# Kernel tuning notes

Hardware: AMD Instinct MI355X
Metric: run time of the kernel (lower is better)

## Reference

```python
import jax, jax.numpy as jnp
import numpy as np
import math

# ---- static configuration (mirrors init_kwargs) ----
NQ = 8            # n_qubits (main register)
NA = 2            # n_ancilla = ceil(log2(n_select))
NSEL = 4          # n_select
DEG = 3           # degree
LAYERS = 2        # n_ansatz_layers
KLOC = 2          # k_local
LATENT = 128
B = 256
NROTS = 4 * NQ * LAYERS          # 64
GROUPS = [(s, s + 1) for s in range(NQ - KLOC + 1)]  # sliding 2-local -> 7 groups
NOBS = len(GROUPS)
KDIM = 2 ** KLOC                  # 4
C64 = jnp.complex64
TWO_PI = 2.0 * math.pi

CNOT = jnp.array([[1, 0, 0, 0], [0, 1, 0, 0], [0, 0, 0, 1], [0, 0, 1, 0]], dtype=C64)

# ---- gate matrices (theta may be traced) ----
def ry_mat(th):
    c = jnp.cos(th / 2).astype(C64); s = jnp.sin(th / 2).astype(C64)
    return jnp.stack([jnp.stack([c, -s]), jnp.stack([s, c])])

def rz_mat(th):
    return jnp.diag(jnp.stack([jnp.exp(-0.5j * th), jnp.exp(0.5j * th)])).astype(C64)

def crx_mat(th):
    c = jnp.cos(th / 2).astype(C64); isn = (-1j * jnp.sin(th / 2)).astype(C64)
    one = jnp.ones((), C64)
    m = jnp.zeros((4, 4), C64)
    m = m.at[0, 0].set(one).at[1, 1].set(one)
    m = m.at[2, 2].set(c).at[3, 3].set(c).at[2, 3].set(isn).at[3, 2].set(isn)
    return m

# ---- state-vector gate application (state: (2,)*rank, wire = axis) ----
def apply_1q(state, U, w):
    return jnp.moveaxis(jnp.tensordot(U, state, axes=((1,), (w,))), 0, w)

def apply_2q(state, U, w0, w1):
    st = jnp.tensordot(U.reshape(2, 2, 2, 2), state, axes=((2, 3), (w0, w1)))
    return jnp.moveaxis(st, (0, 1), (w0, w1))

def _sim14_ops(nq, layers):
    ops, idx = [], 0
    for _ in range(layers):
        for i in range(nq):
            ops.append(("ry", (i,), idx)); idx += 1
        for i in range(nq - 1, -1, -1):
            ops.append(("crx", (i, (i + 1) % nq), idx)); idx += 1
        for i in range(nq):
            ops.append(("ry", (i,), idx)); idx += 1
        for i in [nq - 1] + list(range(nq - 1)):
            ops.append(("crx", (i, (i - 1) % nq), idx)); idx += 1
    return ops

def apply_sim14(state, p, layers, adjoint=False):
    ops = _sim14_ops(NQ, layers)
    seq = list(reversed(ops)) if adjoint else ops
    sgn = -1.0 if adjoint else 1.0
    for kind, ws, idx in seq:
        th = sgn * p[idx]
        if kind == "ry":
            state = apply_1q(state, ry_mat(th), ws[0])
        else:
            state = apply_2q(state, crx_mat(th), ws[0], ws[1])
    return state

def pcphase(state, phi):
    # e^{+i phi} on ancilla=|0..0> subspace (first 2^NQ states in (anc, main) ordering), e^{-i phi} elsewhere
    sr = state.reshape(2 ** NQ, 2 ** NA)
    ph = jnp.where(jnp.arange(2 ** NA) == 0, jnp.exp(1j * phi), jnp.exp(-1j * phi)).astype(C64)
    return (sr * ph[None, :]).reshape(state.shape)

def prepare(state, prep_p, adjoint=False):
    if not adjoint:
        for ly in range(NA):          # n_prep_layers == n_ancilla
            for qi in range(NA):
                state = apply_1q(state, ry_mat(prep_p[ly, qi, 0]), NQ + qi)
                state = apply_1q(state, rz_mat(prep_p[ly, qi, 1]), NQ + qi)
            for i in range(NA - 1):
                state = apply_2q(state, CNOT, NQ + i, NQ + i + 1)
    else:
        for ly in reversed(range(NA)):
            for i in reversed(range(NA - 1)):
                state = apply_2q(state, CNOT, NQ + i, NQ + i + 1)
            for qi in reversed(range(NA)):
                state = apply_1q(state, rz_mat(-prep_p[ly, qi, 1]), NQ + qi)
                state = apply_1q(state, ry_mat(-prep_p[ly, qi, 0]), NQ + qi)
    return state

def select(state, ts, adjoint=False):
    # ancilla wires (NQ, NQ+1) are the trailing axes; flattened index == control value s
    sr = state.reshape((2,) * NQ + (2 ** NA,))
    for s in range(NSEL):
        sub = apply_sim14(sr[..., s], ts[s], LAYERS, adjoint=adjoint)
        sr = sr.at[..., s].set(sub)
    return sr.reshape(state.shape)

def create_hermitian(A, Bp, D, N):
    h = jnp.zeros((N, N), C64)
    count = 0
    for i in range(1, N):
        h = h.at[i - 1, i - 1].set(D[i].astype(C64))
        for j in range(i):
            h = h.at[i, j].set((A[count + j] + 1j * Bp[count + j]).astype(C64))
        count += i
    return h + h.conj().T

def simulate(ts, prep_p, sig, qff, H_all):
    # ts: (NSEL, NROTS) for one batch element
    state = jnp.zeros((2,) * (NQ + NA), C64).at[(0,) * (NQ + NA)].set(1.0)
    state = pcphase(state, sig[0])
    for k in range(DEG):
        state = prepare(state, prep_p)
        state = select(state, ts, adjoint=(k % 2 == 1))
        state = prepare(state, prep_p, adjoint=True)
        state = pcphase(state, sig[k + 1])
    state = apply_sim14(state, qff, 1)
    es = []
    for w, (a, b) in enumerate(GROUPS):
        hpsi = apply_2q(state, H_all[w], a, b)
        es.append(jnp.real(jnp.vdot(state, hpsi)))
    return jnp.stack(es).astype(jnp.float32)  # (NOBS,)

def linear(x, w, b):
    return x @ w.T + b

def sinusoidal_embedding(t, dim):
    half = dim // 2
    freqs = jnp.exp(-math.log(10000.0) * jnp.arange(half, dtype=jnp.float32) / half)
    args = t[:, None] * freqs[None]
    return jnp.concatenate([jnp.cos(args), jnp.sin(args)], axis=-1)

def _forward(z_t, t, te_w1, te_b1, te_w2, te_b2, ip_w1, ip_b1, ip_w2, ip_b2,
             prep_params, signal_angles, qff_params, A_obs, B_obs, D_obs, head_w, head_b):
    t_emb = sinusoidal_embedding(t, LATENT)
    t_emb = linear(jax.nn.silu(linear(t_emb, te_w1, te_b1)), te_w2, te_b2)
    h = jnp.concatenate([z_t, t_emb], axis=-1)
    h = linear(jax.nn.silu(linear(h, ip_w1, ip_b1)), ip_w2, ip_b2)
    ts = jax.nn.sigmoid(h).reshape(z_t.shape[0], NSEL, NROTS) * TWO_PI
    H_all = jax.vmap(lambda a, b, d: create_hermitian(a, b, d, KDIM))(A_obs, B_obs, D_obs)  # (NOBS,4,4)
    expvals = jax.vmap(simulate, in_axes=(0, None, None, None, None))(
        ts, prep_params, signal_angles, qff_params, H_all)  # (B, NOBS)
    return linear(expvals, head_w, head_b)  # (B, LATENT)

def setup_inputs() -> dict:
    key = jax.random.key(0)
    ks = jax.random.split(key, 16)
    def n(k, shape, s=0.05):
        return s * jax.random.normal(k, shape, jnp.float32)
    return {
        "z_t": jax.random.normal(ks[0], (B, LATENT), jnp.float32),
        "t": jax.random.uniform(ks[1], (B,), jnp.float32),
        "te_w1": n(ks[2], (LATENT, LATENT)), "te_b1": jnp.zeros((LATENT,), jnp.float32),
        "te_w2": n(ks[3], (LATENT, LATENT)), "te_b2": jnp.zeros((LATENT,), jnp.float32),
        "ip_w1": n(ks[4], (2 * LATENT, 2 * LATENT)), "ip_b1": jnp.zeros((2 * LATENT,), jnp.float32),
        "ip_w2": n(ks[5], (NSEL * NROTS, 2 * LATENT)), "ip_b2": jnp.zeros((NSEL * NROTS,), jnp.float32),
        "prep_params": 0.1 * jax.random.normal(ks[6], (NA, NA, 2), jnp.float32),
        "signal_angles": 0.1 * jax.random.normal(ks[7], (DEG + 1,), jnp.float32),
        "qff_params": jax.random.uniform(ks[8], (4 * NQ,), jnp.float32),
        "A_obs": 2.0 * jax.random.normal(ks[9], (NOBS, KDIM * (KDIM - 1) // 2), jnp.float32),
        "B_obs": 2.0 * jax.random.normal(ks[10], (NOBS, KDIM * (KDIM - 1) // 2), jnp.float32),
        "D_obs": 2.0 * jax.random.normal(ks[11], (NOBS, KDIM), jnp.float32),
        "head_w": n(ks[12], (LATENT, NOBS)), "head_b": jnp.zeros((LATENT,), jnp.float32),
    }

def reference(z_t, t, te_w1, te_b1, te_w2, te_b2, ip_w1, ip_b1, ip_w2, ip_b2,
              prep_params, signal_angles, qff_params, A_obs, B_obs, D_obs, head_w, head_b):
    return _forward(z_t, t, te_w1, te_b1, te_w2, te_b2, ip_w1, ip_b1, ip_w2, ip_b2,
                    prep_params, signal_angles, qff_params, A_obs, B_obs, D_obs, head_w, head_b)
```

## Files before the change

kernel.cpp:

```cpp
#include <hip/hip_runtime.h>
#include <math.h>

#define NOBS 7
#define PI_F 3.14159265358979f


template<int LM>
__device__ __forceinline__ float lane_partner(float x) {
  if constexpr (LM == 1) {
    return __int_as_float(__builtin_amdgcn_mov_dpp(__float_as_int(x), 0xB1, 0xF, 0xF, true));
  } else if constexpr (LM == 2) {
    return __int_as_float(__builtin_amdgcn_mov_dpp(__float_as_int(x), 0x4E, 0xF, 0xF, true));
  } else if constexpr (LM == 4) {
    int a = __builtin_amdgcn_mov_dpp(__float_as_int(x), 0x1B, 0xF, 0xF, true);
    return __int_as_float(__builtin_amdgcn_mov_dpp(a, 0x141, 0xF, 0xF, true));
  } else if constexpr (LM == 8) {
    int a = __builtin_amdgcn_mov_dpp(__float_as_int(x), 0x141, 0xF, 0xF, true);
    return __int_as_float(__builtin_amdgcn_mov_dpp(a, 0x140, 0xF, 0xF, true));
  } else if constexpr (LM == 16) {
#if __has_builtin(__builtin_amdgcn_permlane16_swap)
    unsigned xu = __float_as_uint(x);
    auto r = __builtin_amdgcn_permlane16_swap(xu, xu, false, false);
    return (__uint_as_float(r[0]) + __uint_as_float(r[1])) - x;
#else
// ... 35 lines not shown

__device__ __forceinline__ float rdlane(float v, int idx) {
  return __int_as_float(__builtin_amdgcn_readlane(__float_as_int(v), idx));
}

__device__ __forceinline__ float2 cmul(float2 a, float2 b) {
  return make_float2(a.x*b.x - a.y*b.y, a.x*b.y + a.y*b.x);
}
__device__ __forceinline__ float2 cmulc(float2 a, float2 b) {
  return make_float2(a.x*b.x + a.y*b.y, a.y*b.x - a.x*b.y);
}
__device__ __forceinline__ float2 cadd(float2 a, float2 b) {
  return make_float2(a.x + b.x, a.y + b.y);
}

struct S4 { float r0, r1, i0, i1; };

__device__ __forceinline__ float4 wexch(int pp, int wv, int lane,
                                        const float* vr, const float* vi) {
  extern __shared__ float4 dxw[];
  float4* buf = dxw + pp * 512;
  buf[wv * 64 + lane] = make_float4(vr[0], vr[1], vi[0], vi[1]);
  __syncthreads();
  return buf[(wv ^ 4) * 64 + lane];
}


template<int W>
__device__ __forceinline__ void ry_lane_g(float* vr, float* vi, int lane,
                                          float ct, float st, int idx, float sg) {
  float c = rdlane(ct, idx), s = sg * rdlane(st, idx);
  constexpr int LM = 1 << (5 - W);
  const float ls = (lane & LM) ? s : -s;
#pragma unroll
  for (int r = 0; r < 2; ++r) {
    float pr = lane_partner<LM>(vr[r]);
    float pi = lane_partner<LM>(vi[r]);
    vr[r] = c*vr[r] + ls*pr;
    vi[r] = c*vi[r] + ls*pi;
  }
}

__device__ __forceinline__ void ry_wave6_g(float* vr, float* vi, int wv, int lane, int h,
                                           float ct, float st, int idx, float sg, int pp) {
  float c = rdlane(ct, idx), s = sg * rdlane(st, idx);
  float4 P = wexch(pp, wv, lane, vr, vi);
  const float ls = h ? s : -s;
  vr[0] = c*vr[0] + ls*P.x;  vr[1] = c*vr[1] + ls*P.y;
  vi[0] = c*vi[0] + ls*P.z;  vi[1] = c*vi[1] + ls*P.w;
}

__device__ __forceinline__ void ry_reg7_g(float* vr, float* vi,
                                          float ct, float st, int idx, float sg) {
  float c = rdlane(ct, idx), s = sg * rdlane(st, idx);
  float a0 = vr[0], a1 = vr[1];
  vr[0] = c*a0 - s*a1;  vr[1] = s*a0 + c*a1;
  float b0 = vi[0], b1 = vi[1];
  vi[0] = c*b0 - s*b1;  vi[1] = s*b0 + c*b1;
}

template<int C, int T>
__device__ __forceinline__ void crx_ll_g(float* vr, float* vi, int lane,
                                         float ct, float st, int idx, float sg) {
  float c = rdlane(ct, idx), s = sg * rdlane(st, idx);
  constexpr int LC = 1 << (5 - C), LT = 1 << (5 - T);
  const bool act = (lane & LC) != 0;
  const float cp = act ? c : 1.f, sp = act ? s : 0.f;
#pragma unroll
  for (int r = 0; r < 2; ++r) {
    float pr = lane_partner<LT>(vr[r]);
    float pi = lane_partner<LT>(vi[r]);
    vr[r] = cp*vr[r] + sp*pi;
    vi[r] = cp*vi[r] - sp*pr;
  }
}

template<int T>
__device__ __forceinline__ void crx_7l_g(float* vr, float* vi,
                                         float ct, float st, int idx, float sg) {
  float c = rdlane(ct, idx), s = sg * rdlane(st, idx);
  constexpr int LT = 1 << (5 - T);
  float pr = lane_partner<LT>(vr[1]);
  float pi = lane_partner<LT>(vi[1]);
  vr[1] = c*vr[1] + s*pi;
  vi[1] = c*vi[1] - s*pr;
}

template<int C>
__device__ __forceinline__ void crx_l7_g(float* vr, float* vi, int lane,
                                         float ct, float st, int idx, float sg) {
  float c = rdlane(ct, idx), s = sg * rdlane(st, idx);
  constexpr int LC = 1 << (5 - C);
  const bool act = (lane & LC) != 0;
  const float cp = act ? c : 1.f, sp = act ? s : 0.f;
  float xr = vr[0], xi = vi[0], yr = vr[1], yi = vi[1];
  vr[0] = cp*xr + sp*yi;  vi[0] = cp*xi - sp*yr;
  vr[1] = cp*yr + sp*xi;  vi[1] = cp*yi - sp*xr;
}

template<int C>
__device__ __forceinline__ void crx_l6_g(float* vr, float* vi, int wv, int lane,
                                         float ct, float st, int idx, float sg, int pp) {
  float c = rdlane(ct, idx), s = sg * rdlane(st, idx);
  float4 P = wexch(pp, wv, lane, vr, vi);
  constexpr int LC = 1 << (5 - C);
  const bool act = (lane & LC) != 0;
  const float cp = act ? c : 1.f, sp = act ? s : 0.f;
  vr[0] = cp*vr[0] + sp*P.z;  vi[0] = cp*vi[0] - sp*P.x;
  vr[1] = cp*vr[1] + sp*P.w;  vi[1] = cp*vi[1] - sp*P.y;
}

__device__ __forceinline__ void crx_76_g(float* vr, float* vi, int wv, int lane,
                                         float ct, float st, int idx, float sg, int pp) {
  float c = rdlane(ct, idx), s = sg * rdlane(st, idx);
  float4 P = wexch(pp, wv, lane, vr, vi);
  vr[1] = c*vr[1] + s*P.w;
  vi[1] = c*vi[1] - s*P.y;
}

__device__ __forceinline__ void crx_67_g(float* vr, float* vi, int h,
                                         float ct, float st, int idx, float sg) {
  if (h) {
    float c = rdlane(ct, idx), s = sg * rdlane(st, idx);
    float xr = vr[0], xi = vi[0], yr = vr[1], yi = vi[1];
    vr[0] = c*xr + s*yi;  vi[0] = c*xi - s*yr;
    vr[1] = c*yr + s*xi;  vi[1] = c*yi - s*xr;
  }
}

template<int T>
__device__ __forceinline__ void crx_6l_g(float* vr, float* vi, int h,
                                         float ct, float st, int idx, float sg) {
  if (h) {
    float c = rdlane(ct, idx), s = sg * rdlane(st, idx);
    constexpr int LT = 1 << (5 - T);
#pragma unroll
    for (int r = 0; r < 2; ++r) {
      float pr = lane_partner<LT>(vr[r]);
      float pi = lane_partner<LT>(vi[r]);
      vr[r] = c*vr[r] + s*pi;
      vi[r] = c*vi[r] - s*pr;
    }
  }
}


__device__ __noinline__ S4 sim14_fwd(S4 v, float ct, float st, int off) {
  const int tid = threadIdx.x;
  const int lane = tid & 63, wv = tid >> 6, h = wv >> 2;
  float vr[2] = {v.r0, v.r1}, vi[2] = {v.i0, v.i1};
  const float sg = 1.f;
  ry_lane_g<0>(vr,vi,lane,ct,st,off+0,sg); ry_lane_g<1>(vr,vi,lane,ct,st,off+1,sg);
  ry_lane_g<2>(vr,vi,lane,ct,st,off+2,sg); ry_lane_g<3>(vr,vi,lane,ct,st,off+3,sg);
  ry_lane_g<4>(vr,vi,lane,ct,st,off+4,sg); ry_lane_g<5>(vr,vi,lane,ct,st,off+5,sg);
  ry_wave6_g(vr,vi,wv,lane,h,ct,st,off+6,sg,0);
  ry_reg7_g(vr,vi,ct,st,off+7,sg);
  crx_7l_g<0>(vr,vi,ct,st,off+8,sg);
  crx_67_g(vr,vi,h,ct,st,off+9,sg);
  crx_l6_g<5>(vr,vi,wv,lane,ct,st,off+10,sg,1);
  crx_ll_g<4,5>(vr,vi,lane,ct,st,off+11,sg); crx_ll_g<3,4>(vr,vi,lane,ct,st,off+12,sg);
  crx_ll_g<2,3>(vr,vi,lane,ct,st,off+13,sg); crx_ll_g<1,2>(vr,vi,lane,ct,st,off+14,sg);
  crx_ll_g<0,1>(vr,vi,lane,ct,st,off+15,sg);
  ry_lane_g<0>(vr,vi,lane,ct,st,off+16,sg); ry_lane_g<1>(vr,vi,lane,ct,st,off+17,sg);
  ry_lane_g<2>(vr,vi,lane,ct,st,off+18,sg); ry_lane_g<3>(vr,vi,lane,ct,st,off+19,sg);
  ry_lane_g<4>(vr,vi,lane,ct,st,off+20,sg); ry_lane_g<5>(vr,vi,lane,ct,st,off+21,sg);
  ry_wave6_g(vr,vi,wv,lane,h,ct,st,off+22,sg,0);
  ry_reg7_g(vr,vi,ct,st,off+23,sg);
  crx_76_g(vr,vi,wv,lane,ct,st,off+24,sg,1);
  crx_l7_g<0>(vr,vi,lane,ct,st,off+25,sg);
  crx_ll_g<1,0>(vr,vi,lane,ct,st,off+26,sg); crx_ll_g<2,1>(vr,vi,lane,ct,st,off+27,sg);
  crx_ll_g<3,2>(vr,vi,lane,ct,st,off+28,sg); crx_ll_g<4,3>(vr,vi,lane,ct,st,off+29,sg);
  crx_ll_g<5,4>(vr,vi,lane,ct,st,off+30,sg);
  crx_6l_g<5>(vr,vi,h,ct,st,off+31,sg);
  return {vr[0], vr[1], vi[0], vi[1]};
}

__device__ __noinline__ S4 sim14_adj(S4 v, float ct, float st, int off) {
  const int tid = threadIdx.x;
  const int lane = tid & 63, wv = tid >> 6, h = wv >> 2;
  float vr[2] = {v.r0, v.r1}, vi[2] = {v.i0, v.i1};
  const float sg = -1.f;
  crx_6l_g<5>(vr,vi,h,ct,st,off+31,sg);
  crx_ll_g<5,4>(vr,vi,lane,ct,st,off+30,sg); crx_ll_g<4,3>(vr,vi,lane,ct,st,off+29,sg);
  crx_ll_g<3,2>(vr,vi,lane,ct,st,off+28,sg); crx_ll_g<2,1>(vr,vi,lane,ct,st,off+27,sg);
  crx_ll_g<1,0>(vr,vi,lane,ct,st,off+26,sg);
  crx_l7_g<0>(vr,vi,lane,ct,st,off+25,sg);
  crx_76_g(vr,vi,wv,lane,ct,st,off+24,sg,0);
  ry_reg7_g(vr,vi,ct,st,off+23,sg);
  ry_wave6_g(vr,vi,wv,lane,h,ct,st,off+22,sg,1);
  ry_lane_g<5>(vr,vi,lane,ct,st,off+21,sg); ry_lane_g<4>(vr,vi,lane,ct,st,off+20,sg);
  ry_lane_g<3>(vr,vi,lane,ct,st,off+19,sg); ry_lane_g<2>(vr,vi,lane,ct,st,off+18,sg);
  ry_lane_g<1>(vr,vi,lane,ct,st,off+17,sg); ry_lane_g<0>(vr,vi,lane,ct,st,off+16,sg);
  crx_ll_g<0,1>(vr,vi,lane,ct,st,off+15,sg); crx_ll_g<1,2>(vr,vi,lane,ct,st,off+14,sg);
  crx_ll_g<2,3>(vr,vi,lane,ct,st,off+13,sg); crx_ll_g<3,4>(vr,vi,lane,ct,st,off+12,sg);
  crx_ll_g<4,5>(vr,vi,lane,ct,st,off+11,sg);
  crx_l6_g<5>(vr,vi,wv,lane,ct,st,off+10,sg,0);
  crx_67_g(vr,vi,h,ct,st,off+9,sg);
  crx_7l_g<0>(vr,vi,ct,st,off+8,sg);
  ry_reg7_g(vr,vi,ct,st,off+7,sg);
  ry_wave6_g(vr,vi,wv,lane,h,ct,st,off+6,sg,1);
  ry_lane_g<5>(vr,vi,lane,ct,st,off+5,sg); ry_lane_g<4>(vr,vi,lane,ct,st,off+4,sg);
  ry_lane_g<3>(vr,vi,lane,ct,st,off+3,sg); ry_lane_g<2>(vr,vi,lane,ct,st,off+2,sg);
  ry_lane_g<1>(vr,vi,lane,ct,st,off+1,sg); ry_lane_g<0>(vr,vi,lane,ct,st,off+0,sg);
  return {vr[0], vr[1], vi[0], vi[1]};
}


__global__ void setup_kernel(const float* __restrict__ prep_p,
                             const float* __restrict__ sig,
                             const float* __restrict__ qff,
                             float* __restrict__ ws) {
  const int t = threadIdx.x;
  float2 Ga[2][2][2], Gb[2][2][2];
  for (int ly = 0; ly < 2; ++ly)
    for (int qi = 0; qi < 2; ++qi) {
      float y = prep_p[ly*4 + qi*2 + 0], z = prep_p[ly*4 + qi*2 + 1];
      float cy, sy, cz, sz;
      __sincosf(0.5f*y, &sy, &cy);
      __sincosf(0.5f*z, &sz, &cz);
// ... 80 lines not shown
      if constexpr (MODE == 0) {
        yl[row] = a / (1.f + __expf(-a));
      } else if constexpr (MODE == 1) {
        yl[row] = a;
      } else {
        float th = PI_F / (1.f + __expf(-a));
        float sn, cn;
        __sincosf(th, &sn, &cn);
        ((float2*)yl)[row] = make_float2(cn, sn);
      }
    }
  }
}


__global__ __launch_bounds__(512) void qsvt_kernel(
    const float* __restrict__ z_t, const float* __restrict__ t,
    const float* __restrict__ te_w1, const float* __restrict__ te_b1,
    const float* __restrict__ te_w2, const float* __restrict__ te_b2,
    const float* __restrict__ ip_w1, const float* __restrict__ ip_b1,
    const float* __restrict__ ip_w2, const float* __restrict__ ip_b2,
    const float* __restrict__ A_obs, const float* __restrict__ B_obs,
    const float* __restrict__ D_obs,
    const float* __restrict__ head_w, const float* __restrict__ head_b,
    const float* __restrict__ ws,
    float* __restrict__ out)
{
  __shared__ __align__(16) float emb[128];
  __shared__ __align__(16) float y1[128];
  __shared__ __align__(16) float hbuf[256];
  __shared__ __align__(16) float h1[256];
  __shared__ __align__(16) float2 seltab[256];
  __shared__ __align__(16) float2 xanc[128 * 9];
  __shared__ __align__(16) float dumpR[4][256];
  __shared__ __align__(16) float dumpI[4][256];
  __shared__ float redbuf[NOBS][4];
  __shared__ float hdc[NOBS][3], hxc[NOBS][6], hyc[NOBS][6];
  __shared__ __align__(16) float shw[128 * NOBS];
  __shared__ __align__(16) float shb[128];

  const int tid  = threadIdx.x;
  const int lane = tid & 63;
  const int wv   = tid >> 6;
  const int s    = wv & 3;
  const int h    = wv >> 2;
  const int b    = blockIdx.x;

  if (tid < 128) {
    float fr = ws[168 + (tid & 63)];
    float arg = t[b] * fr;
    float sn, cn;
    __sincosf(arg, &sn, &cn);
    emb[tid] = (tid < 64) ? cn : sn;
  }
  __syncthreads();

  mlp_layer<128, 2, 0>(te_w1, te_b1, emb, y1, wv * 16, lane);
  if (tid < 128) hbuf[tid] = z_t[b * 128 + tid];
  __syncthreads();

  mlp_layer<128, 2, 1>(te_w2, te_b2, y1, hbuf + 128, wv * 16, lane);
  __syncthreads();

  mlp_layer<256, 4, 0>(ip_w1, ip_b1, hbuf, h1, wv * 32, lane);
  __syncthreads();

  mlp_layer<256, 4, 2>(ip_w2, ip_b2, h1, (float*)seltab, wv * 32, lane);

  if (tid < NOBS * 6)      { hxc[tid/6][tid%6] = A_obs[tid]; hyc[tid/6][tid%6] = B_obs[tid]; }
  else if (tid >= 64 && tid < 64 + NOBS*3) { int q = tid - 64; hdc[q/3][q%3] = 2.f * D_obs[(q/3)*4 + (q%3) + 1]; }
#pragma unroll
  for (int i = tid; i < 128*NOBS; i += 512) shw[i] = head_w[i];
  if (tid < 128) shb[tid] = head_b[tid];
  __syncthreads();

  float2 mycs = seltab[(s << 6) | lane];
  float selc = mycs.x, sels = mycs.y;
  float2 myq = ((const float2*)(ws + 104))[lane & 31];
  float qc = myq.x, qs = myq.y;

  S4 v;
  v.r0 = 0.f; v.r1 = 0.f; v.i0 = 0.f; v.i1 = 0.f;
  if (lane == 0 && h == 0) {
    float2 a0 = ((const float2*)(ws + 96))[s];
    v.r0 = a0.x; v.i0 = a0.y;
  }

  const int ancbase = (h * 64 + lane) * 9;

  v = sim14_fwd(v, selc, sels, 0);
  v = sim14_fwd(v, selc, sels, 32);
  {
    const float2* R = (const float2*)ws + (s << 2);
    xanc[ancbase + 0 + s] = make_float2(v.r0, v.i0);
    xanc[ancbase + 4 + s] = make_float2(v.r1, v.i1);
    __syncthreads();
    float2 o0 = cmul(R[0], xanc[ancbase + 0]);
    o0 = cadd(o0, cmul(R[1], xanc[ancbase + 1]));
    o0 = cadd(o0, cmul(R[2], xanc[ancbase + 2]));
    o0 = cadd(o0, cmul(R[3], xanc[ancbase + 3]));
    float2 o1 = cmul(R[0], xanc[ancbase + 4]);
    o1 = cadd(o1, cmul(R[1], xanc[ancbase + 5]));
    o1 = cadd(o1, cmul(R[2], xanc[ancbase + 6]));
    o1 = cadd(o1, cmul(R[3], xanc[ancbase + 7]));
    v.r0 = o0.x; v.i0 = o0.y; v.r1 = o1.x; v.i1 = o1.y;
    __syncthreads();
  }
  v = sim14_adj(v, selc, sels, 32);
  v = sim14_adj(v, selc, sels, 0);
  {
    const float2* R = (const float2*)(ws + 32) + (s << 2);
    xanc[ancbase + 0 + s] = make_float2(v.r0, v.i0);
    xanc[ancbase + 4 + s] = make_float2(v.r1, v.i1);
    __syncthreads();
    float2 o0 = cmul(R[0], xanc[ancbase + 0]);
    o0 = cadd(o0, cmul(R[1], xanc[ancbase + 1]));
    o0 = cadd(o0, cmul(R[2], xanc[ancbase + 2]));
    o0 = cadd(o0, cmul(R[3], xanc[ancbase + 3]));
    float2 o1 = cmul(R[0], xanc[ancbase + 4]);
    o1 = cadd(o1, cmul(R[1], xanc[ancbase + 5]));
    o1 = cadd(o1, cmul(R[2], xanc[ancbase + 6]));
    o1 = cadd(o1, cmul(R[3], xanc[ancbase + 7]));
    v.r0 = o0.x; v.i0 = o0.y; v.r1 = o1.x; v.i1 = o1.y;
    __syncthreads();
  }
  v = sim14_fwd(v, selc, sels, 0);
  v = sim14_fwd(v, selc, sels, 32);
  {
    const float2* R = (const float2*)(ws + 64) + (s << 2);
    xanc[ancbase + 0 + s] = make_float2(v.r0, v.i0);
    xanc[ancbase + 4 + s] = make_float2(v.r1, v.i1);
    __syncthreads();
    float2 o0 = cmul(R[0], xanc[ancbase + 0]);
    o0 = cadd(o0, cmul(R[1], xanc[ancbase + 1]));
    o0 = cadd(o0, cmul(R[2], xanc[ancbase + 2]));
    o0 = cadd(o0, cmul(R[3], xanc[ancbase + 3]));
    float2 o1 = cmul(R[0], xanc[ancbase + 4]);
    o1 = cadd(o1, cmul(R[1], xanc[ancbase + 5]));
    o1 = cadd(o1, cmul(R[2], xanc[ancbase + 6]));
    o1 = cadd(o1, cmul(R[3], xanc[ancbase + 7]));
    v.r0 = o0.x; v.i0 = o0.y; v.r1 = o1.x; v.i1 = o1.y;
    __syncthreads();
  }
  v = sim14_fwd(v, qc, qs, 0);

  *(float2*)&dumpR[s][(lane << 2) | (h << 1)] = make_float2(v.r0, v.r1);
  *(float2*)&dumpI[s][(lane << 2) | (h << 1)] = make_float2(v.i0, v.i1);
  __syncthreads();

  const int w0 = h ? 4 : 0, w1 = h ? NOBS : 4;
  for (int w = w0; w < w1; ++w) {
    const int pb = 6 - w;
    int g = lane;
    int ib = ((g >> pb) << (pb + 2)) | (g & ((1 << pb) - 1));
    float xr[4], xi[4];
#pragma unroll
    for (int i = 0; i < 4; ++i) { xr[i] = dumpR[s][ib + (i << pb)]; xi[i] = dumpI[s][ib + (i << pb)]; }
    float a = hdc[w][0] * (xr[0]*xr[0] + xi[0]*xi[0])
            + hdc[w][1] * (xr[1]*xr[1] + xi[1]*xi[1])
            + hdc[w][2] * (xr[2]*xr[2] + xi[2]*xi[2]);
    const int oi[6] = {1, 2, 2, 3, 3, 3};
    const int oj[6] = {0, 0, 1, 0, 1, 2};
#pragma unroll
    for (int k2 = 0; k2 < 6; ++k2) {
      int i = oi[k2], j = oj[k2];
      float rr = xr[i]*xr[j] + xi[i]*xi[j];
      float ii = xr[i]*xi[j] - xi[i]*xr[j];
      a += 2.f * (hxc[w][k2]*rr - hyc[w][k2]*ii);
    }
    a = xor_sum<32>(a);
    a = xor_sum<16>(a);
    a = xor_sum<8>(a);
    a = xor_sum<4>(a);
    a = xor_sum<2>(a);
    a = xor_sum<1>(a);
    if (lane == 0) redbuf[w][s] = a;
  }
  __syncthreads();

  if (tid < 128) {
    float acc = shb[tid];
#pragma unroll
    for (int w = 0; w < NOBS; ++w) {
      float ev = redbuf[w][0] + redbuf[w][1] + redbuf[w][2] + redbuf[w][3];
      acc += ev * shw[tid*NOBS + w];
    }
    out[b * 128 + tid] = acc;
  }
}

extern "C" void kernel_launch(void* const* d_in, const int* in_sizes, int n_in,
                              void* d_out, int out_size, void* d_ws, size_t ws_size,
                              hipStream_t stream) {
  (void)n_in; (void)out_size; (void)ws_size;
  const float* z_t    = (const float*)d_in[0];
  const float* t      = (const float*)d_in[1];
  const float* te_w1  = (const float*)d_in[2];
  const float* te_b1  = (const float*)d_in[3];
  const float* te_w2  = (const float*)d_in[4];
// ... 4 lines not shown
  const float* ip_b2  = (const float*)d_in[9];
  const float* prep_p = (const float*)d_in[10];
  const float* sig    = (const float*)d_in[11];
  const float* qff    = (const float*)d_in[12];
  const float* A_obs  = (const float*)d_in[13];
  const float* B_obs  = (const float*)d_in[14];
  const float* D_obs  = (const float*)d_in[15];
  const float* head_w = (const float*)d_in[16];
  const float* head_b = (const float*)d_in[17];
  float* out = (float*)d_out;
  float* ws  = (float*)d_ws;

  setup_kernel<<<1, 64, 0, stream>>>(prep_p, sig, qff, ws);

  int B = in_sizes[1];
  qsvt_kernel<<<B, 512, 2 * 512 * sizeof(float4), stream>>>(
      z_t, t, te_w1, te_b1, te_w2, te_b2, ip_w1, ip_b1, ip_w2, ip_b2,
      A_obs, B_obs, D_obs, head_w, head_b, ws, out);
}
```

Baseline: 127.4 us.

## Double block size to one amplitude per thread with padded LDS exchange

The block grows from 512 to 1024 threads, so each thread holds one complex amplitude instead of two. Qubits 6 and 7 now live across wave groups, and the two RY rotations on them are fused into one LDS exchange with a padded stride of 17 to avoid bank conflicts. Exchanges alternate between two buffers, the MLP layers are re-split across 16 waves, and the observable reduction is spread over more waves. This doubles parallelism per sample, but the added cross-wave gates need more block-wide barriers, and those barriers across 16 waves may cost more than the extra threads save.

```diff
diff --git a/kernel.cpp b/kernel.cpp
--- a/kernel.cpp
+++ b/kernel.cpp
@@ -73,195 +73,201 @@
   return make_float2(a.x + b.x, a.y + b.y);
 }
 
-struct S4 { float r0, r1, i0, i1; };
-
-__device__ __forceinline__ float4 wexch(int pp, int wv, int lane,
-                                        const float* vr, const float* vi) {
-  extern __shared__ float4 dxw[];
-  float4* buf = dxw + pp * 512;
-  buf[wv * 64 + lane] = make_float4(vr[0], vr[1], vi[0], vi[1]);
-  __syncthreads();
-  return buf[(wv ^ 4) * 64 + lane];
-}
-
-
-template<int W>
-__device__ __forceinline__ void ry_lane_g(float* vr, float* vi, int lane,
-                                          float ct, float st, int idx, float sg) {
-  float c = rdlane(ct, idx), s = sg * rdlane(st, idx);
-  constexpr int LM = 1 << (5 - W);
-  const float ls = (lane & LM) ? s : -s;
-#pragma unroll
-  for (int r = 0; r < 2; ++r) {
-    float pr = lane_partner<LM>(vr[r]);
-    float pi = lane_partner<LM>(vi[r]);
-    vr[r] = c*vr[r] + ls*pr;
-    vi[r] = c*vi[r] + ls*pi;
-  }
-}
-
-__device__ __forceinline__ void ry_wave6_g(float* vr, float* vi, int wv, int lane, int h,
-                                           float ct, float st, int idx, float sg, int pp) {
-  float c = rdlane(ct, idx), s = sg * rdlane(st, idx);
-  float4 P = wexch(pp, wv, lane, vr, vi);
-  const float ls = h ? s : -s;
-  vr[0] = c*vr[0] + ls*P.x;  vr[1] = c*vr[1] + ls*P.y;
-  vi[0] = c*vi[0] + ls*P.z;  vi[1] = c*vi[1] + ls*P.w;
-}
-
-__device__ __forceinline__ void ry_reg7_g(float* vr, float* vi,
-                                          float ct, float st, int idx, float sg) {
-  float c = rdlane(ct, idx), s = sg * rdlane(st, idx);
-  float a0 = vr[0], a1 = vr[1];
-  vr[0] = c*a0 - s*a1;  vr[1] = s*a0 + c*a1;
-  float b0 = vi[0], b1 = vi[1];
-  vi[0] = c*b0 - s*b1;  vi[1] = s*b0 + c*b1;
-}
-
-template<int C, int T>
-__device__ __forceinline__ void crx_ll_g(float* vr, float* vi, int lane,
-                                         float ct, float st, int idx, float sg) {
-  float c = rdlane(ct, idx), s = sg * rdlane(st, idx);
-  constexpr int LC = 1 << (5 - C), LT = 1 << (5 - T);
-  const bool act = (lane & LC) != 0;
-  const float cp = act ? c : 1.f, sp = act ? s : 0.f;
-#pragma unroll
-  for (int r = 0; r < 2; ++r) {
-    float pr = lane_partner<LT>(vr[r]);
-    float pi = lane_partner<LT>(vi[r]);
-    vr[r] = cp*vr[r] + sp*pi;
-    vi[r] = cp*vi[r] - sp*pr;
-  }
-}
-
-template<int T>
-__device__ __forceinline__ void crx_7l_g(float* vr, float* vi,
-                                         float ct, float st, int idx, float sg) {
-  float c = rdlane(ct, idx), s = sg * rdlane(st, idx);
-  constexpr int LT = 1 << (5 - T);
-  float pr = lane_partner<LT>(vr[1]);
-  float pi = lane_partner<LT>(vi[1]);
-  vr[1] = c*vr[1] + s*pi;
-  vi[1] = c*vi[1] - s*pr;
-}
-
-template<int C>
-__device__ __forceinline__ void crx_l7_g(float* vr, float* vi, int lane,
-                                         float ct, float st, int idx, float sg) {
-  float c = rdlane(ct, idx), s = sg * rdlane(st, idx);
-  constexpr int LC = 1 << (5 - C);
-  const bool act = (lane & LC) != 0;
-  const float cp = act ? c : 1.f, sp = act ? s : 0.f;
-  float xr = vr[0], xi = vi[0], yr = vr[1], yi = vi[1];
-  vr[0] = cp*xr + sp*yi;  vi[0] = cp*xi - sp*yr;
-  vr[1] = cp*yr + sp*xi;  vi[1] = cp*yi - sp*xr;
-}
-
-template<int C>
-__device__ __forceinline__ void crx_l6_g(float* vr, float* vi, int wv, int lane,
-                                         float ct, float st, int idx, float sg, int pp) {
-  float c = rdlane(ct, idx), s = sg * rdlane(st, idx);
-  float4 P = wexch(pp, wv, lane, vr, vi);
-  constexpr int LC = 1 << (5 - C);
-  const bool act = (lane & LC) != 0;
-  const float cp = act ? c : 1.f, sp = act ? s : 0.f;
-  vr[0] = cp*vr[0] + sp*P.z;  vi[0] = cp*vi[0] - sp*P.x;
-  vr[1] = cp*vr[1] + sp*P.w;  vi[1] = cp*vi[1] - sp*P.y;
-}
-
-__device__ __forceinline__ void crx_76_g(float* vr, float* vi, int wv, int lane,
-                                         float ct, float st, int idx, float sg, int pp) {
-  float c = rdlane(ct, idx), s = sg * rdlane(st, idx);
-  float4 P = wexch(pp, wv, lane, vr, vi);
-  vr[1] = c*vr[1] + s*P.w;
-  vi[1] = c*vi[1] - s*P.y;
-}
-
-__device__ __forceinline__ void crx_67_g(float* vr, float* vi, int h,
-                                         float ct, float st, int idx, float sg) {
-  if (h) {
-    float c = rdlane(ct, idx), s = sg * rdlane(st, idx);
-    float xr = vr[0], xi = vi[0], yr = vr[1], yi = vi[1];
-    vr[0] = c*xr + s*yi;  vi[0] = c*xi - s*yr;
-    vr[1] = c*yr + s*xi;  vi[1] = c*yi - s*xr;
-  }
-}
-
-template<int T>
-__device__ __forceinline__ void crx_6l_g(float* vr, float* vi, int h,
-                                         float ct, float st, int idx, float sg) {
-  if (h) {
-    float c = rdlane(ct, idx), s = sg * rdlane(st, idx);
-    constexpr int LT = 1 << (5 - T);
-#pragma unroll
-    for (int r = 0; r < 2; ++r) {
-      float pr = lane_partner<LT>(vr[r]);
-      float pi = lane_partner<LT>(vi[r]);
-      vr[r] = c*vr[r] + s*pi;
-      vi[r] = c*vi[r] - s*pr;
-    }
-  }
-}
-
-
-__device__ __noinline__ S4 sim14_fwd(S4 v, float ct, float st, int off) {
+struct S2 { float r, i; };
+
+#define XSLOTS 1088
+
+
+__device__ __noinline__ S2 sim14_fwd(S2 v, float ct, float st, int off, int site0) {
+  extern __shared__ float2 dxw[];
   const int tid = threadIdx.x;
-  const int lane = tid & 63, wv = tid >> 6, h = wv >> 2;
-  float vr[2] = {v.r0, v.r1}, vi[2] = {v.i0, v.i1};
+  const int lane = tid & 63, wv = tid >> 6;
+  const int s = wv & 3, q = wv >> 2;
+  const int h6 = q & 1, h7 = q >> 1;
+  const int sb = lane * 17 + s * 4;
+  float vr = v.r, vi = v.i;
   const float sg = 1.f;
-  ry_lane_g<0>(vr,vi,lane,ct,st,off+0,sg); ry_lane_g<1>(vr,vi,lane,ct,st,off+1,sg);
-  ry_lane_g<2>(vr,vi,lane,ct,st,off+2,sg); ry_lane_g<3>(vr,vi,lane,ct,st,off+3,sg);
-  ry_lane_g<4>(vr,vi,lane,ct,st,off+4,sg); ry_lane_g<5>(vr,vi,lane,ct,st,off+5,sg);
-  ry_wave6_g(vr,vi,wv,lane,h,ct,st,off+6,sg,0);
-  ry_reg7_g(vr,vi,ct,st,off+7,sg);
-  crx_7l_g<0>(vr,vi,ct,st,off+8,sg);
-  crx_67_g(vr,vi,h,ct,st,off+9,sg);
-  crx_l6_g<5>(vr,vi,wv,lane,ct,st,off+10,sg,1);
-  crx_ll_g<4,5>(vr,vi,lane,ct,st,off+11,sg); crx_ll_g<3,4>(vr,vi,lane,ct,st,off+12,sg);
-  crx_ll_g<2,3>(vr,vi,lane,ct,st,off+13,sg); crx_ll_g<1,2>(vr,vi,lane,ct,st,off+14,sg);
-  crx_ll_g<0,1>(vr,vi,lane,ct,st,off+15,sg);
-  ry_lane_g<0>(vr,vi,lane,ct,st,off+16,sg); ry_lane_g<1>(vr,vi,lane,ct,st,off+17,sg);
-  ry_lane_g<2>(vr,vi,lane,ct,st,off+18,sg); ry_lane_g<3>(vr,vi,lane,ct,st,off+19,sg);
-  ry_lane_g<4>(vr,vi,lane,ct,st,off+20,sg); ry_lane_g<5>(vr,vi,lane,ct,st,off+21,sg);
-  ry_wave6_g(vr,vi,wv,lane,h,ct,st,off+22,sg,0);
-  ry_reg7_g(vr,vi,ct,st,off+23,sg);
-  crx_76_g(vr,vi,wv,lane,ct,st,off+24,sg,1);
-  crx_l7_g<0>(vr,vi,lane,ct,st,off+25,sg);
-  crx_ll_g<1,0>(vr,vi,lane,ct,st,off+26,sg); crx_ll_g<2,1>(vr,vi,lane,ct,st,off+27,sg);
-  crx_ll_g<3,2>(vr,vi,lane,ct,st,off+28,sg); crx_ll_g<4,3>(vr,vi,lane,ct,st,off+29,sg);
-  crx_ll_g<5,4>(vr,vi,lane,ct,st,off+30,sg);
-  crx_6l_g<5>(vr,vi,h,ct,st,off+31,sg);
-  return {vr[0], vr[1], vi[0], vi[1]};
-}
-
-__device__ __noinline__ S4 sim14_adj(S4 v, float ct, float st, int off) {
+
+  auto RYL = [&](auto Wc, int idx) {
+    constexpr int LM = 1 << (5 - decltype(Wc)::value);
+    float c = rdlane(ct, idx), ss = sg * rdlane(st, idx);
+    float ls = (lane & LM) ? ss : -ss;
+    float pr = lane_partner<LM>(vr), pi = lane_partner<LM>(vi);
+    vr = c*vr + ls*pr;  vi = c*vi + ls*pi;
+  };
+  auto QUAD = [&](int i6, int i7, int site) {
+    float c6 = rdlane(ct, i6), s6 = sg * rdlane(st, i6);
+    float c7 = rdlane(ct, i7), s7 = sg * rdlane(st, i7);
+    float r60 = h6 ? s6 : c6, r61 = h6 ? c6 : -s6;
+    float r70 = h7 ? s7 : c7, r71 = h7 ? c7 : -s7;
+    float2* buf = dxw + (site & 1) * XSLOTS;
+    buf[sb + q] = make_float2(vr, vi);
+    __syncthreads();
+    float2 p0 = buf[sb+0], p1 = buf[sb+1], p2 = buf[sb+2], p3 = buf[sb+3];
+    float f0 = r60*r70, f1 = r61*r70, f2 = r60*r71, f3 = r61*r71;
+    vr = f0*p0.x + f1*p1.x + f2*p2.x + f3*p3.x;
+    vi = f0*p0.y + f1*p1.y + f2*p2.y + f3*p3.y;
+  };
+  auto CRXLL = [&](auto Cc, auto Tc, int idx) {
+    constexpr int LC = 1 << (5 - decltype(Cc)::value);
+    constexpr int LT = 1 << (5 - decltype(Tc)::value);
+    float c = rdlane(ct, idx), ss = sg * rdlane(st, idx);
+    bool act = (lane & LC) != 0;
+    float cp = act ? c : 1.f, sp = act ? ss : 0.f;
+    float pr = lane_partner<LT>(vr), pi = lane_partner<LT>(vi);
+    vr = cp*vr + sp*pi;  vi = cp*vi - sp*pr;
+  };
+  auto CRXUL = [&](int hact, auto Tc, int idx) {
+    if (hact) {
+      constexpr int LT = 1 << (5 - decltype(Tc)::value);
+      float c = rdlane(ct, idx), ss = sg * rdlane(st, idx);
+      float pr = lane_partner<LT>(vr), pi = lane_partner<LT>(vi);
+      vr = c*vr + ss*pi;  vi = c*vi - ss*pr;
+    }
+  };
+  auto CRXUW = [&](int hact, int qmask, int idx, int site) {
+    float2* buf = dxw + (site & 1) * XSLOTS;
+    if (hact) buf[sb + q] = make_float2(vr, vi);
+    __syncthreads();
+    if (hact) {
+      float c = rdlane(ct, idx), ss = sg * rdlane(st, idx);
+      float2 P = buf[sb + (q ^ qmask)];
+      vr = c*vr + ss*P.y;  vi = c*vi - ss*P.x;
+    }
+  };
+  auto CRXLW = [&](auto Cc, int qmask, int idx, int site) {
+    constexpr int LC = 1 << (5 - decltype(Cc)::value);
+    float c = rdlane(ct, idx), ss = sg * rdlane(st, idx);
+    float2* buf = dxw + (site & 1) * XSLOTS;
+    buf[sb + q] = make_float2(vr, vi);
+    __syncthreads();
+    float2 P = buf[sb + (q ^ qmask)];
+    bool act = (lane & LC) != 0;
+    float cp = act ? c : 1.f, sp = act ? ss : 0.f;
+    vr = cp*vr + sp*P.y;  vi = cp*vi - sp*P.x;
+  };
+
+  RYL(std::integral_constant<int,0>{}, off+0); RYL(std::integral_constant<int,1>{}, off+1);
+  RYL(std::integral_constant<int,2>{}, off+2); RYL(std::integral_constant<int,3>{}, off+3);
+  RYL(std::integral_constant<int,4>{}, off+4); RYL(std::integral_constant<int,5>{}, off+5);
+  QUAD(off+6, off+7, site0+0);
+  CRXUL(h7, std::integral_constant<int,0>{}, off+8);
+  CRXUW(h6, 2, off+9,  site0+1);
+  CRXLW(std::integral_constant<int,5>{}, 1, off+10, site0+2);
+  CRXLL(std::integral_constant<int,4>{}, std::integral_constant<int,5>{}, off+11);
+  CRXLL(std::integral_constant<int,3>{}, std::integral_constant<int,4>{}, off+12);
+  CRXLL(std::integral_constant<int,2>{}, std::integral_constant<int,3>{}, off+13);
+  CRXLL(std::integral_constant<int,1>{}, std::integral_constant<int,2>{}, off+14);
+  CRXLL(std::integral_constant<int,0>{}, std::integral_constant<int,1>{}, off+15);
+  RYL(std::integral_constant<int,0>{}, off+16); RYL(std::integral_constant<int,1>{}, off+17);
+  RYL(std::integral_constant<int,2>{}, off+18); RYL(std::integral_constant<int,3>{}, off+19);
+  RYL(std::integral_constant<int,4>{}, off+20); RYL(std::integral_constant<int,5>{}, off+21);
+  QUAD(off+22, off+23, site0+3);
+  CRXUW(h7, 1, off+24, site0+4);
+  CRXLW(std::integral_constant<int,0>{}, 2, off+25, site0+5);
+  CRXLL(std::integral_constant<int,1>{}, std::integral_constant<int,0>{}, off+26);
+  CRXLL(std::integral_constant<int,2>{}, std::integral_constant<int,1>{}, off+27);
+  CRXLL(std::integral_constant<int,3>{}, std::integral_constant<int,2>{}, off+28);
+  CRXLL(std::integral_constant<int,4>{}, std::integral_constant<int,3>{}, off+29);
+  CRXLL(std::integral_constant<int,5>{}, std::integral_constant<int,4>{}, off+30);
+  CRXUL(h6, std::integral_constant<int,5>{}, off+31);
+  return {vr, vi};
+}
+
+__device__ __noinline__ S2 sim14_adj(S2 v, float ct, float st, int off, int site0) {
+  extern __shared__ float2 dxw[];
   const int tid = threadIdx.x;
-  const int lane = tid & 63, wv = tid >> 6, h = wv >> 2;
-  float vr[2] = {v.r0, v.r1}, vi[2] = {v.i0, v.i1};
+  const int lane = tid & 63, wv = tid >> 6;
+  const int s = wv & 3, q = wv >> 2;
+  const int h6 = q & 1, h7 = q >> 1;
+  const int sb = lane * 17 + s * 4;
+  float vr = v.r, vi = v.i;
   const float sg = -1.f;
-  crx_6l_g<5>(vr,vi,h,ct,st,off+31,sg);
-  crx_ll_g<5,4>(vr,vi,lane,ct,st,off+30,sg); crx_ll_g<4,3>(vr,vi,lane,ct,st,off+29,sg);
-  crx_ll_g<3,2>(vr,vi,lane,ct,st,off+28,sg); crx_ll_g<2,1>(vr,vi,lane,ct,st,off+27,sg);
-  crx_ll_g<1,0>(vr,vi,lane,ct,st,off+26,sg);
-  crx_l7_g<0>(vr,vi,lane,ct,st,off+25,sg);
-  crx_76_g(vr,vi,wv,lane,ct,st,off+24,sg,0);
-  ry_reg7_g(vr,vi,ct,st,off+23,sg);
-  ry_wave6_g(vr,vi,wv,lane,h,ct,st,off+22,sg,1);
-  ry_lane_g<5>(vr,vi,lane,ct,st,off+21,sg); ry_lane_g<4>(vr,vi,lane,ct,st,off+20,sg);
-  ry_lane_g<3>(vr,vi,lane,ct,st,off+19,sg); ry_lane_g<2>(vr,vi,lane,ct,st,off+18,sg);
-  ry_lane_g<1>(vr,vi,lane,ct,st,off+17,sg); ry_lane_g<0>(vr,vi,lane,ct,st,off+16,sg);
-  crx_ll_g<0,1>(vr,vi,lane,ct,st,off+15,sg); crx_ll_g<1,2>(vr,vi,lane,ct,st,off+14,sg);
-  crx_ll_g<2,3>(vr,vi,lane,ct,st,off+13,sg); crx_ll_g<3,4>(vr,vi,lane,ct,st,off+12,sg);
-  crx_ll_g<4,5>(vr,vi,lane,ct,st,off+11,sg);
-  crx_l6_g<5>(vr,vi,wv,lane,ct,st,off+10,sg,0);
-  crx_67_g(vr,vi,h,ct,st,off+9,sg);
-  crx_7l_g<0>(vr,vi,ct,st,off+8,sg);
-  ry_reg7_g(vr,vi,ct,st,off+7,sg);
-  ry_wave6_g(vr,vi,wv,lane,h,ct,st,off+6,sg,1);
-  ry_lane_g<5>(vr,vi,lane,ct,st,off+5,sg); ry_lane_g<4>(vr,vi,lane,ct,st,off+4,sg);
-  ry_lane_g<3>(vr,vi,lane,ct,st,off+3,sg); ry_lane_g<2>(vr,vi,lane,ct,st,off+2,sg);
-  ry_lane_g<1>(vr,vi,lane,ct,st,off+1,sg); ry_lane_g<0>(vr,vi,lane,ct,st,off+0,sg);
-  return {vr[0], vr[1], vi[0], vi[1]};
+
+  auto RYL = [&](auto Wc, int idx) {
+    constexpr int LM = 1 << (5 - decltype(Wc)::value);
+    float c = rdlane(ct, idx), ss = sg * rdlane(st, idx);
+    float ls = (lane & LM) ? ss : -ss;
+    float pr = lane_partner<LM>(vr), pi = lane_partner<LM>(vi);
+    vr = c*vr + ls*pr;  vi = c*vi + ls*pi;
+  };
+  auto QUAD = [&](int i6, int i7, int site) {
+    float c6 = rdlane(ct, i6), s6 = sg * rdlane(st, i6);
+    float c7 = rdlane(ct, i7), s7 = sg * rdlane(st, i7);
+    float r60 = h6 ? s6 : c6, r61 = h6 ? c6 : -s6;
+    float r70 = h7 ? s7 : c7, r71 = h7 ? c7 : -s7;
+    float2* buf = dxw + (site & 1) * XSLOTS;
+    buf[sb + q] = make_float2(vr, vi);
+    __syncthreads();
+    float2 p0 = buf[sb+0], p1 = buf[sb+1], p2 = buf[sb+2], p3 = buf[sb+3];
+    float f0 = r60*r70, f1 = r61*r70, f2 = r60*r71, f3 = r61*r71;
+    vr = f0*p0.x + f1*p1.x + f2*p2.x + f3*p3.x;
+    vi = f0*p0.y + f1*p1.y + f2*p2.y + f3*p3.y;
+  };
+  auto CRXLL = [&](auto Cc, auto Tc, int idx) {
+    constexpr int LC = 1 << (5 - decltype(Cc)::value);
+    constexpr int LT = 1 << (5 - decltype(Tc)::value);
+    float c = rdlane(ct, idx), ss = sg * rdlane(st, idx);
+    bool act = (lane & LC) != 0;
+    float cp = act ? c : 1.f, sp = act ? ss : 0.f;
+    float pr = lane_partner<LT>(vr), pi = lane_partner<LT>(vi);
+    vr = cp*vr + sp*pi;  vi = cp*vi - sp*pr;
+  };
+  auto CRXUL = [&](int hact, auto Tc, int idx) {
+    if (hact) {
+      constexpr int LT = 1 << (5 - decltype(Tc)::value);
+      float c = rdlane(ct, idx), ss = sg * rdlane(st, idx);
+      float pr = lane_partner<LT>(vr), pi = lane_partner<LT>(vi);
+      vr = c*vr + ss*pi;  vi = c*vi - ss*pr;
+    }
+  };
+  auto CRXUW = [&](int hact, int qmask, int idx, int site) {
+    float2* buf = dxw + (site & 1) * XSLOTS;
+    if (hact) buf[sb + q] = make_float2(vr, vi);
+    __syncthreads();
+    if (hact) {
+      float c = rdlane(ct, idx), ss = sg * rdlane(st, idx);
+      float2 P = buf[sb + (q ^ qmask)];
+      vr = c*vr + ss*P.y;  vi = c*vi - ss*P.x;
+    }
+  };
+  auto CRXLW = [&](auto Cc, int qmask, int idx, int site) {
+    constexpr int LC = 1 << (5 - decltype(Cc)::value);
+    float c = rdlane(ct, idx), ss = sg * rdlane(st, idx);
+    float2* buf = dxw + (site & 1) * XSLOTS;
+    buf[sb + q] = make_float2(vr, vi);
+    __syncthreads();
+    float2 P = buf[sb + (q ^ qmask)];
+    bool act = (lane & LC) != 0;
+    float cp = act ? c : 1.f, sp = act ? ss : 0.f;
+    vr = cp*vr + sp*P.y;  vi = cp*vi - sp*P.x;
+  };
+
+  CRXUL(h6, std::integral_constant<int,5>{}, off+31);
+  CRXLL(std::integral_constant<int,5>{}, std::integral_constant<int,4>{}, off+30);
+  CRXLL(std::integral_constant<int,4>{}, std::integral_constant<int,3>{}, off+29);
+  CRXLL(std::integral_constant<int,3>{}, std::integral_constant<int,2>{}, off+28);
+  CRXLL(std::integral_constant<int,2>{}, std::integral_constant<int,1>{}, off+27);
+  CRXLL(std::integral_constant<int,1>{}, std::integral_constant<int,0>{}, off+26);
+  CRXLW(std::integral_constant<int,0>{}, 2, off+25, site0+0);
+  CRXUW(h7, 1, off+24, site0+1);
+  QUAD(off+22, off+23, site0+2);
+  RYL(std::integral_constant<int,5>{}, off+21); RYL(std::integral_constant<int,4>{}, off+20);
+  RYL(std::integral_constant<int,3>{}, off+19); RYL(std::integral_constant<int,2>{}, off+18);
+  RYL(std::integral_constant<int,1>{}, off+17); RYL(std::integral_constant<int,0>{}, off+16);
+  CRXLL(std::integral_constant<int,0>{}, std::integral_constant<int,1>{}, off+15);
+  CRXLL(std::integral_constant<int,1>{}, std::integral_constant<int,2>{}, off+14);
+  CRXLL(std::integral_constant<int,2>{}, std::integral_constant<int,3>{}, off+13);
+  CRXLL(std::integral_constant<int,3>{}, std::integral_constant<int,4>{}, off+12);
+  CRXLL(std::integral_constant<int,4>{}, std::integral_constant<int,5>{}, off+11);
+  CRXLW(std::integral_constant<int,5>{}, 1, off+10, site0+3);
+  CRXUW(h6, 2, off+9, site0+4);
+  CRXUL(h7, std::integral_constant<int,0>{}, off+8);
+  QUAD(off+6, off+7, site0+5);
+  RYL(std::integral_constant<int,5>{}, off+5); RYL(std::integral_constant<int,4>{}, off+4);
+  RYL(std::integral_constant<int,3>{}, off+3); RYL(std::integral_constant<int,2>{}, off+2);
+  RYL(std::integral_constant<int,1>{}, off+1); RYL(std::integral_constant<int,0>{}, off+0);
+  return {vr, vi};
 }
 
 
@@ -372,7 +378,7 @@
 }
 
 
-__global__ __launch_bounds__(512) void qsvt_kernel(
+__global__ __launch_bounds__(1024) void qsvt_kernel(
     const float* __restrict__ z_t, const float* __restrict__ t,
     const float* __restrict__ te_w1, const float* __restrict__ te_b1,
     const float* __restrict__ te_w2, const float* __restrict__ te_b2,
@@ -389,19 +395,21 @@
   __shared__ __align__(16) float hbuf[256];
   __shared__ __align__(16) float h1[256];
   __shared__ __align__(16) float2 seltab[256];
-  __shared__ __align__(16) float2 xanc[128 * 9];
   __shared__ __align__(16) float dumpR[4][256];
   __shared__ __align__(16) float dumpI[4][256];
-  __shared__ float redbuf[NOBS][4];
+  __shared__ float redbuf[NOBS][2];
   __shared__ float hdc[NOBS][3], hxc[NOBS][6], hyc[NOBS][6];
   __shared__ __align__(16) float shw[128 * NOBS];
   __shared__ __align__(16) float shb[128];
+  extern __shared__ float2 dxw[];
 
   const int tid  = threadIdx.x;
   const int lane = tid & 63;
   const int wv   = tid >> 6;
   const int s    = wv & 3;
-  const int h    = wv >> 2;
+  const int q    = wv >> 2;
+  const int h6   = q & 1;
+  const int h7   = q >> 1;
   const int b    = blockIdx.x;
 
   if (tid < 128) {
@@ -413,22 +421,22 @@
   }
   __syncthreads();
 
-  mlp_layer<128, 2, 0>(te_w1, te_b1, emb, y1, wv * 16, lane);
+  mlp_layer<128, 1, 0>(te_w1, te_b1, emb, y1, wv * 8, lane);
   if (tid < 128) hbuf[tid] = z_t[b * 128 + tid];
   __syncthreads();
 
-  mlp_layer<128, 2, 1>(te_w2, te_b2, y1, hbuf + 128, wv * 16, lane);
-  __syncthreads();
-
-  mlp_layer<256, 4, 0>(ip_w1, ip_b1, hbuf, h1, wv * 32, lane);
-  __syncthreads();
-
-  mlp_layer<256, 4, 2>(ip_w2, ip_b2, h1, (float*)seltab, wv * 32, lane);
+  mlp_layer<128, 1, 1>(te_w2, te_b2, y1, hbuf + 128, wv * 8, lane);
+  __syncthreads();
+
+  mlp_layer<256, 2, 0>(ip_w1, ip_b1, hbuf, h1, wv * 16, lane);
+  __syncthreads();
+
+  mlp_layer<256, 2, 2>(ip_w2, ip_b2, h1, (float*)seltab, wv * 16, lane);
 
   if (tid < NOBS * 6)      { hxc[tid/6][tid%6] = A_obs[tid]; hyc[tid/6][tid%6] = B_obs[tid]; }
-  else if (tid >= 64 && tid < 64 + NOBS*3) { int q = tid - 64; hdc[q/3][q%3] = 2.f * D_obs[(q/3)*4 + (q%3) + 1]; }
-#pragma unroll
-  for (int i = tid; i < 128*NOBS; i += 512) shw[i] = head_w[i];
+  else if (tid >= 64 && tid < 64 + NOBS*3) { int qd = tid - 64; hdc[qd/3][qd%3] = 2.f * D_obs[(qd/3)*4 + (qd%3) + 1]; }
+#pragma unroll
+  for (int i = tid; i < 128*NOBS; i += 1024) shw[i] = head_w[i];
   if (tid < 128) shb[tid] = head_b[tid];
   __syncthreads();
 
@@ -437,102 +445,97 @@
   float2 myq = ((const float2*)(ws + 104))[lane & 31];
   float qc = myq.x, qs = myq.y;
 
-  S4 v;
-  v.r0 = 0.f; v.r1 = 0.f; v.i0 = 0.f; v.i1 = 0.f;
-  if (lane == 0 && h == 0) {
+  S2 v;
+  v.r = 0.f; v.i = 0.f;
+  if (lane == 0 && q == 0) {
     float2 a0 = ((const float2*)(ws + 96))[s];
-    v.r0 = a0.x; v.i0 = a0.y;
-  }
-
-  const int ancbase = (h * 64 + lane) * 9;
-
-  v = sim14_fwd(v, selc, sels, 0);
-  v = sim14_fwd(v, selc, sels, 32);
+    v.r = a0.x; v.i = a0.y;
+  }
+
+  const int sb = lane * 17 + s * 4;
+
+  v = sim14_fwd(v, selc, sels, 0, 0);
+  v = sim14_fwd(v, selc, sels, 32, 6);
   {
     const float2* R = (const float2*)ws + (s << 2);
-    xanc[ancbase + 0 + s] = make_float2(v.r0, v.i0);
-    xanc[ancbase + 4 + s] = make_float2(v.r1, v.i1);
-    __syncthreads();
-    float2 o0 = cmul(R[0], xanc[ancbase + 0]);
-    o0 = cadd(o0, cmul(R[1], xanc[ancbase + 1]));
-    o0 = cadd(o0, cmul(R[2], xanc[ancbase + 2]));
-    o0 = cadd(o0, cmul(R[3], xanc[ancbase + 3]));
-    float2 o1 = cmul(R[0], xanc[ancbase + 4]);
-    o1 = cadd(o1, cmul(R[1], xanc[ancbase + 5]));
-    o1 = cadd(o1, cmul(R[2], xanc[ancbase + 6]));
-    o1 = cadd(o1, cmul(R[3], xanc[ancbase + 7]));
-    v.r0 = o0.x; v.i0 = o0.y; v.r1 = o1.x; v.i1 = o1.y;
-    __syncthreads();
-  }
-  v = sim14_adj(v, selc, sels, 32);
-  v = sim14_adj(v, selc, sels, 0);
+    float2* buf = dxw + (12 & 1) * XSLOTS;
+    buf[sb + q] = make_float2(v.r, v.i);
+    __syncthreads();
+    float2 o = cmul(R[0], buf[lane*17 + 0*4 + q]);
+    o = cadd(o, cmul(R[1], buf[lane*17 + 1*4 + q]));
+    o = cadd(o, cmul(R[2], buf[lane*17 + 2*4 + q]));
+    o = cadd(o, cmul(R[3], buf[lane*17 + 3*4 + q]));
+    v.r = o.x; v.i = o.y;
+  }
+  v = sim14_adj(v, selc, sels, 32, 13);
+  v = sim14_adj(v, selc, sels, 0, 19);
   {
     const float2* R = (const float2*)(ws + 32) + (s << 2);
-    xanc[ancbase + 0 + s] = make_float2(v.r0, v.i0);
-    xanc[ancbase + 4 + s] = make_float2(v.r1, v.i1);
-    __syncthreads();
-    float2 o0 = cmul(R[0], xanc[ancbase + 0]);
-    o0 = cadd(o0, cmul(R[1], xanc[ancbase + 1]));
-    o0 = cadd(o0, cmul(R[2], xanc[ancbase + 2]));
-    o0 = cadd(o0, cmul(R[3], xanc[ancbase + 3]));
-    float2 o1 = cmul(R[0], xanc[ancbase + 4]);
-    o1 = cadd(o1, cmul(R[1], xanc[ancbase + 5]));
-    o1 = cadd(o1, cmul(R[2], xanc[ancbase + 6]));
-    o1 = cadd(o1, cmul(R[3], xanc[ancbase + 7]));
-    v.r0 = o0.x; v.i0 = o0.y; v.r1 = o1.x; v.i1 = o1.y;
-    __syncthreads();
-  }
-  v = sim14_fwd(v, selc, sels, 0);
-  v = sim14_fwd(v, selc, sels, 32);
+    float2* buf = dxw + (25 & 1) * XSLOTS;
+    buf[sb + q] = make_float2(v.r, v.i);
+    __syncthreads();
+    float2 o = cmul(R[0], buf[lane*17 + 0*4 + q]);
+    o = cadd(o, cmul(R[1], buf[lane*17 + 1*4 + q]));
+    o = cadd(o, cmul(R[2], buf[lane*17 + 2*4 + q]));
+    o = cadd(o, cmul(R[3], buf[lane*17 + 3*4 + q]));
+    v.r = o.x; v.i = o.y;
+  }
+  v = sim14_fwd(v, selc, sels, 0, 26);
+  v = sim14_fwd(v, selc, sels, 32, 32);
   {
     const float2* R = (const float2*)(ws + 64) + (s << 2);
-    xanc[ancbase + 0 + s] = make_float2(v.r0, v.i0);
-    xanc[ancbase + 4 + s] = make_float2(v.r1, v.i1);
-    __syncthreads();
-    float2 o0 = cmul(R[0], xanc[ancbase + 0]);
-    o0 = cadd(o0, cmul(R[1], xanc[ancbase + 1]));
-    o0 = cadd(o0, cmul(R[2], xanc[ancbase + 2]));
-    o0 = cadd(o0, cmul(R[3], xanc[ancbase + 3]));
-    float2 o1 = cmul(R[0], xanc[ancbase + 4]);
-    o1 = cadd(o1, cmul(R[1], xanc[ancbase + 5]));
-    o1 = cadd(o1, cmul(R[2], xanc[ancbase + 6]));
-    o1 = cadd(o1, cmul(R[3], xanc[ancbase + 7]));
-    v.r0 = o0.x; v.i0 = o0.y; v.r1 = o1.x; v.i1 = o1.y;
-    __syncthreads();
-  }
-  v = sim14_fwd(v, qc, qs, 0);
-
-  *(float2*)&dumpR[s][(lane << 2) | (h << 1)] = make_float2(v.r0, v.r1);
-  *(float2*)&dumpI[s][(lane << 2) | (h << 1)] = make_float2(v.i0, v.i1);
-  __syncthreads();
-
-  const int w0 = h ? 4 : 0, w1 = h ? NOBS : 4;
-  for (int w = w0; w < w1; ++w) {
-    const int pb = 6 - w;
-    int g = lane;
-    int ib = ((g >> pb) << (pb + 2)) | (g & ((1 << pb) - 1));
-    float xr[4], xi[4];
-#pragma unroll
-    for (int i = 0; i < 4; ++i) { xr[i] = dumpR[s][ib + (i << pb)]; xi[i] = dumpI[s][ib + (i << pb)]; }
-    float a = hdc[w][0] * (xr[0]*xr[0] + xi[0]*xi[0])
-            + hdc[w][1] * (xr[1]*xr[1] + xi[1]*xi[1])
-            + hdc[w][2] * (xr[2]*xr[2] + xi[2]*xi[2]);
-    const int oi[6] = {1, 2, 2, 3, 3, 3};
-    const int oj[6] = {0, 0, 1, 0, 1, 2};
-#pragma unroll
-    for (int k2 = 0; k2 < 6; ++k2) {
-      int i = oi[k2], j = oj[k2];
-      float rr = xr[i]*xr[j] + xi[i]*xi[j];
-      float ii = xr[i]*xi[j] - xi[i]*xr[j];
-      a += 2.f * (hxc[w][k2]*rr - hyc[w][k2]*ii);
-    }
-    a = xor_sum<32>(a);
-    a = xor_sum<16>(a);
-    a = xor_sum<8>(a);
-    a = xor_sum<4>(a);
-    a = xor_sum<2>(a);
-    a = xor_sum<1>(a);
-    if (lane == 0) redbuf[w][s] = a;
+    float2* buf = dxw + (38 & 1) * XSLOTS;
+    buf[sb + q] = make_float2(v.r, v.i);
+    __syncthreads();
+    float2 o = cmul(R[0], buf[lane*17 + 0*4 + q]);
+    o = cadd(o, cmul(R[1], buf[lane*17 + 1*4 + q]));
+    o = cadd(o, cmul(R[2], buf[lane*17 + 2*4 + q]));
+    o = cadd(o, cmul(R[3], buf[lane*17 + 3*4 + q]));
+    v.r = o.x; v.i = o.y;
+  }
+  v = sim14_fwd(v, qc, qs, 0, 39);
+
+  {
+    int m = (lane << 2) | (h6 << 1) | h7;
+    dumpR[s][m] = v.r;
+    dumpI[s][m] = v.i;
+  }
+  __syncthreads();
+
+  {
+    const int w = wv & 7, sh = wv >> 3;
+    if (w < NOBS) {
+      const int pb = 6 - w;
+      int g = lane;
+      int ib = ((g >> pb) << (pb + 2)) | (g & ((1 << pb) - 1));
+      float a = 0.f;
+#pragma unroll
+      for (int si = 0; si < 2; ++si) {
+        const int s2 = sh * 2 + si;
+        float xr[4], xi[4];
+#pragma unroll
+        for (int i = 0; i < 4; ++i) { xr[i] = dumpR[s2][ib + (i << pb)]; xi[i] = dumpI[s2][ib + (i << pb)]; }
+        a += hdc[w][0] * (xr[0]*xr[0] + xi[0]*xi[0])
+           + hdc[w][1] * (xr[1]*xr[1] + xi[1]*xi[1])
+           + hdc[w][2] * (xr[2]*xr[2] + xi[2]*xi[2]);
+        const int oi[6] = {1, 2, 2, 3, 3, 3};
+        const int oj[6] = {0, 0, 1, 0, 1, 2};
+#pragma unroll
+        for (int k2 = 0; k2 < 6; ++k2) {
+          int i = oi[k2], j = oj[k2];
+          float rr = xr[i]*xr[j] + xi[i]*xi[j];
+          float ii = xr[i]*xi[j] - xi[i]*xr[j];
+          a += 2.f * (hxc[w][k2]*rr - hyc[w][k2]*ii);
+        }
+      }
+      a = xor_sum<32>(a);
+      a = xor_sum<16>(a);
+      a = xor_sum<8>(a);
+      a = xor_sum<4>(a);
+      a = xor_sum<2>(a);
+      a = xor_sum<1>(a);
+      if (lane == 0) redbuf[w][sh] = a;
+    }
   }
   __syncthreads();
 
@@ -540,7 +543,7 @@
     float acc = shb[tid];
 #pragma unroll
     for (int w = 0; w < NOBS; ++w) {
-      float ev = redbuf[w][0] + redbuf[w][1] + redbuf[w][2] + redbuf[w][3];
+      float ev = redbuf[w][0] + redbuf[w][1];
       acc += ev * shw[tid*NOBS + w];
     }
     out[b * 128 + tid] = acc;
@@ -575,7 +578,8 @@
   setup_kernel<<<1, 64, 0, stream>>>(prep_p, sig, qff, ws);
 
   int B = in_sizes[1];
-  qsvt_kernel<<<B, 512, 2 * 512 * sizeof(float4), stream>>>(
+  size_t dyn = 2 * XSLOTS * sizeof(float2);
+  qsvt_kernel<<<B, 1024, dyn, stream>>>(
       z_t, t, te_w1, te_b1, te_w2, te_b2, ip_w1, ip_b1, ip_w2, ip_b2,
       A_obs, B_obs, D_obs, head_w, head_b, ws, out);
 }
```

Result: slower. 131.3 us (+3.1%).
